# Kernel tuning notes

Measured on AMD Instinct MI355X. Metric: run time of the kernel, lower is better.

Reference implementation:

```python
import jax, jax.numpy as jnp
import numpy as np

B, NC, NT = 1, 128, 256
F = 8                       # fidnet filters (both 1h and 13c)
KH, KW = 5, 8               # fidnet kernel
DILS = [1, 2, 3, 4, 6, 8, 10, 12, 14, 16, 18, 20, 24, 28, 32]
BLOCKS = 3
L = BLOCKS * len(DILS)      # 45 wave layers per FIDNetLayer
RSTEPS, RK = 4, 9           # refine steps / refine kernel


def dfh_tanh(x):
    return jnp.tanh(x) * 0.98 + x * 0.02


def dfh_sigmoid(x):
    return jax.nn.sigmoid(x) * 0.98 + x * 0.02


def dfh_relu(x):
    return jax.nn.relu(x) * 0.98 + x * 0.02


def conv2d(x, w, b, dil_w=1, padding='VALID'):
    # x: NHWC, w: HWIO
    out = jax.lax.conv_general_dilated(x, w, (1, 1), padding,
                                       rhs_dilation=(1, dil_w),
                                       dimension_numbers=('NHWC', 'HWIO', 'NHWC'))
    return out + b


def hilbert(x):
    # analytic signal along last axis (real input, even length)
    N = x.shape[-1]
    hh = jnp.concatenate([jnp.ones(1, jnp.float32), 2.0 * jnp.ones(N // 2 - 1, jnp.float32),
                          jnp.ones(1, jnp.float32), jnp.zeros(N // 2 - 1, jnp.float32)]).astype(jnp.complex64)
    return jnp.fft.ifft(jnp.fft.fft(x.astype(jnp.complex64)) * hh)


def fidnet_layer(x, dw, db, wy1, by1, wy2, by2, wz0, bz0):
    # WaveNet-style stack of gated dilated convs with residuals + skip sum
    x = dfh_tanh(x @ dw + db)            # (B,H,W,2F)
    skip = jnp.zeros_like(x)
    ph = (KH - 1) // 2
    for i in range(wy1.shape[0]):
        dil = DILS[i % len(DILS)]
        xin = jnp.pad(x, ((0, 0), (ph, ph), (0, dil * (KW - 1)), (0, 0)))
        y1 = dfh_tanh(conv2d(xin, wy1[i], by1[i], dil))
        y2 = dfh_sigmoid(conv2d(xin, wy2[i], by2[i], dil))
        z = jnp.pad(y1 * y2, ((0, 0), (ph, ph), (0, KW - 1), (0, 0)))
        z = conv2d(z, wz0[i], bz0[i], 1)
        skip = skip + z
        x = z + x
    return dfh_tanh(skip)


def setup_inputs():
    key = jax.random.key(0)
    ks = jax.random.split(key, 16)
    n = lambda k, s, sc=0.05: jax.random.normal(k, s, jnp.float32) * sc
    return {
        'times': n(ks[0], (B, 2, NT), 1.0),
        'times_in': n(ks[1], (B, NC), 1.0),
        'inp_2d_nc': n(ks[2], (B, 1, NC, NT), 1.0),
        'inp_2d_c': n(ks[3], (B, 1, NC, NT), 1.0),
        'c_dense_w': n(ks[4], (4, 2 * F)), 'c_dense_b': jnp.zeros((2 * F,), jnp.float32),
        'c_wy1': n(ks[5], (L, KH, KW, 2 * F, F)), 'c_by1': jnp.zeros((L, F), jnp.float32),
        'c_wy2': n(ks[6], (L, KH, KW, 2 * F, F)), 'c_by2': jnp.zeros((L, F), jnp.float32),
        'c_wz0': n(ks[7], (L, KH, KW, F, 2 * F)), 'c_bz0': jnp.zeros((L, 2 * F), jnp.float32),
        'h_dense_w': n(ks[8], (2 * F, 2 * F)), 'h_dense_b': jnp.zeros((2 * F,), jnp.float32),
        'h_wy1': n(ks[9], (L, KH, KW, 2 * F, F)), 'h_by1': jnp.zeros((L, F), jnp.float32),
        'h_wy2': n(ks[10], (L, KH, KW, 2 * F, F)), 'h_by2': jnp.zeros((L, F), jnp.float32),
        'h_wz0': n(ks[11], (L, KH, KW, F, 2 * F)), 'h_bz0': jnp.zeros((L, 2 * F), jnp.float32),
        'ref_wr': n(ks[12], (RSTEPS, RK, RK, 8 * F, 4 * F), 0.02), 'ref_br': jnp.zeros((RSTEPS, 4 * F), jnp.float32),
        'ref_wt': n(ks[13], (RSTEPS, RK, RK, 8 * F, 4 * F), 0.02), 'ref_bt': jnp.zeros((RSTEPS, 4 * F), jnp.float32),
        'dense_w': n(ks[14], (12 * F, 2)), 'dense_b': jnp.zeros((2,), jnp.float32),
    }


def reference(times, times_in, inp_2d_nc, inp_2d_c,
              c_dense_w, c_dense_b, c_wy1, c_by1, c_wy2, c_by2, c_wz0, c_bz0,
              h_dense_w, h_dense_b, h_wy1, h_by1, h_wy2, h_by2, h_wz0, h_bz0,
              ref_wr, ref_br, ref_wt, ref_bt, dense_w, dense_b):
    Bn, _, nc, nt = inp_2d_nc.shape
    # build 4-channel input plane (B, NT, NC, 4)
    times_plane = jnp.tile(times[:, :1, :], (1, nc, 1))[:, None]          # (B,1,NC,NT)
    times_in_plane = jnp.tile(times_in[:, :, None], (1, 1, nt))[:, None]  # (B,1,NC,NT)
    tr = lambda a: jnp.transpose(a, (0, 3, 2, 1))
    inp = jnp.concatenate([tr(inp_2d_nc), tr(inp_2d_c), tr(times_plane), tr(times_in_plane)], axis=-1)

    cout = fidnet_layer(inp, c_dense_w, c_dense_b, c_wy1, c_by1, c_wy2, c_by2, c_wz0, c_bz0)  # (B,NT,NC,2F)
    cout = jnp.transpose(cout, (0, 3, 1, 2))               # (B,2F,NT,NC)
    cout = jnp.pad(cout, ((0, 0), (0, 0), (0, 0), (0, nc)))  # (B,2F,NT,2NC)
    mult = jnp.concatenate([jnp.full((1,), 0.5, jnp.float32), jnp.ones(nc - 1, jnp.float32)])
    multc = mult.astype(jnp.complex64)
    cout_ft = jnp.fft.fftshift(jnp.fft.fft(multc * (cout[..., 0::2] + 1j * cout[..., 1::2])), axes=-1)
    cout_ft = jnp.transpose(jnp.real(cout_ft), (0, 1, 3, 2))  # (B,2F,NC,NT)
    cout_ft = hilbert(cout_ft)
    hinp = jnp.conj(jnp.fft.fft(jnp.fft.fftshift(cout_ft, axes=-1)) / nt)
    mult_pad = jnp.pad(mult, (0, nt - nc), constant_values=1.0).astype(jnp.complex64)
    hinp = hinp / mult_pad
    zero_mask = jnp.where(jnp.abs(times[:, 0, 2::2]) > 0.0, 1.0, 0.0)
    zero_mask = jnp.pad(zero_mask, ((0, 0), (1, 0)), constant_values=1.0)[:, None, None, :]  # (B,1,1,NT//2)
    hinp = hinp[..., :nt // 2] * zero_mask
    hinp = jnp.stack([jnp.real(hinp), jnp.imag(hinp)], axis=-1).reshape(Bn, 2 * F, nc, nt)
    hinp = jnp.transpose(hinp, (0, 2, 3, 1)).astype(jnp.float32)  # (B,NC,NT,2F)

    hout = fidnet_layer(hinp, h_dense_w, h_dense_b, h_wy1, h_by1, h_wy2, h_by2, h_wz0, h_bz0)
    hout = jnp.concatenate([hout, hinp], axis=-1)          # (B,NC,NT,4F)
    hout = jnp.transpose(hout, (0, 3, 1, 2))               # (B,4F,NC,NT)
    hout = jnp.pad(hout, ((0, 0), (0, 0), (0, 0), (0, nt)))
    winH = jnp.concatenate([jnp.full((1,), 0.5, jnp.float32), jnp.ones(nt - 1, jnp.float32)]).astype(jnp.complex64)
    hout_ft = jnp.fft.fftshift(jnp.fft.fft(winH * (hout[..., 0::2] + 1j * hout[..., 1::2])), axes=-1)
    hout_ft = jnp.transpose(jnp.real(hout_ft), (0, 2, 3, 1))  # (B,NC,NT,4F)

    fnorm = jnp.max(jnp.abs(hout_ft), axis=(1, 2, 3), keepdims=True)
    ref = jnp.tile(hout_ft / fnorm, (1, 1, 1, 2))          # (B,NC,NT,8F)
    for i in range(ref_wr.shape[0]):
        rr = dfh_relu(conv2d(ref, ref_wr[i], ref_br[i], 1, 'SAME'))
        tt = dfh_tanh(conv2d(ref, ref_wt[i], ref_bt[i], 1, 'SAME'))
        ref = jnp.concatenate([tt, rr], axis=-1) + ref
    ref = ref * fnorm
    hfin = jnp.concatenate([ref, hout_ft], axis=-1) @ dense_w + dense_b  # (B,NC,NT,2)
    return jnp.stack([hfin[..., 0], hfin[..., 1] / fnorm[..., 0]], axis=-1)
```

## Files before the change

kernel.cpp:

```cpp
#include <hip/hip_runtime.h>

#define NTT 256
#define NCC 128

typedef __attribute__((ext_vector_type(8))) short bf16x8;
typedef __attribute__((ext_vector_type(4))) float f32x4;

__device__ __forceinline__ float dfh_tanh_f(float v){ return tanhf(v)*0.98f + 0.02f*v; }
__device__ __forceinline__ float dfh_sig_f(float v){ return 0.98f/(1.f+expf(-v)) + 0.02f*v; }
__device__ __forceinline__ unsigned f2bf(float x){
  unsigned u = __float_as_uint(x);
  return (u + 0x7fffu + ((u>>16)&1u)) >> 16;
}

__global__ __launch_bounds__(256) void k_build_c(
    const float* __restrict__ times, const float* __restrict__ times_in,
    const float* __restrict__ i2nc, const float* __restrict__ i2c,
    const float* __restrict__ dw, const float* __restrict__ db,
    float* __restrict__ x, unsigned short* __restrict__ xb,
    float* __restrict__ skip)
{
  int gid = blockIdx.x*256 + threadIdx.x;
  if (gid >= NTT*NCC) return;
  int c = gid & 127, t = gid >> 7;
  float v0 = i2nc[c*NTT + t];
  float v1 = i2c [c*NTT + t];
  float v2 = times[t];
  float v3 = times_in[c];
  #pragma unroll
  for (int f=0; f<16; ++f){
    float a = v0*dw[f] + v1*dw[16+f] + v2*dw[32+f] + v3*dw[48+f] + db[f];
    float xv = dfh_tanh_f(a);
    x[gid*16+f]    = xv;
    xb[gid*16+f]   = (unsigned short)f2bf(xv);
    skip[gid*16+f] = 0.f;
  }
}

__global__ __launch_bounds__(256) void k_build_h(
    const float* __restrict__ hinp, const float* __restrict__ dw,
    const float* __restrict__ db, float* __restrict__ x,
    unsigned short* __restrict__ xb, float* __restrict__ skip)
{
  int gid = blockIdx.x*256 + threadIdx.x;
  if (gid >= NCC*NTT) return;
  const float* in = hinp + gid*16;
  float iv[16];
  #pragma unroll
  for (int i=0;i<16;i++) iv[i]=in[i];
  #pragma unroll
  for (int f=0; f<16; ++f){
    float a = db[f];
    #pragma unroll
    for (int i=0;i<16;i++) a += iv[i]*dw[i*16+f];
    float xv = dfh_tanh_f(a);
    x[gid*16+f]    = xv;
    xb[gid*16+f]   = (unsigned short)f2bf(xv);
    skip[gid*16+f] = 0.f;
  }
}

__global__ __launch_bounds__(256) void k_wpack(
    const float* __restrict__ cwy1, const float* __restrict__ cwy2,
    const float* __restrict__ cwz0,
    const float* __restrict__ hwy1, const float* __restrict__ hwy2,
    const float* __restrict__ hwz0,
    unsigned short* __restrict__ gfrag, unsigned short* __restrict__ zfrag)
{
  int tid = blockIdx.x*256 + threadIdx.x;
  if (tid < 115200){
    int lane = tid & 63, ks = (tid>>6) % 20, layer = tid / 1280;
    const float* w1 = (layer < 45) ? cwy1 + layer*5120 : hwy1 + (layer-45)*5120;
    const float* w2 = (layer < 45) ? cwy2 + layer*5120 : hwy2 + (layer-45)*5120;
    int n = lane & 15;
    unsigned pk[4];
    #pragma unroll
    for (int jj=0; jj<4; ++jj){
      unsigned hl[2];
      #pragma unroll
      for (int h2=0; h2<2; ++h2){
        int k = ks*32 + (lane>>4)*8 + jj*2 + h2;
        int tap = k>>4, ci = k&15;
        float v = (n<8) ? w1[(tap*16+ci)*8 + n] : w2[(tap*16+ci)*8 + (n-8)];
        hl[h2] = f2bf(v);
      }
      pk[jj] = hl[0] | (hl[1]<<16);
    }
    uint4 v4; v4.x=pk[0]; v4.y=pk[1]; v4.z=pk[2]; v4.w=pk[3];
    *reinterpret_cast<uint4*>(gfrag + (size_t)tid*8) = v4;
  } else if (tid < 172800){
    int t2 = tid - 115200;
    int lane = t2 & 63, ks = (t2>>6) % 10, layer = t2 / 640;
    const float* wz = (layer < 45) ? cwz0 + layer*5120 : hwz0 + (layer-45)*5120;
    int n = lane & 15;
    unsigned pk[4];
    #pragma unroll
    for (int jj=0; jj<4; ++jj){
      unsigned hl[2];
      #pragma unroll
      for (int h2=0; h2<2; ++h2){
        int k = ks*32 + (lane>>4)*8 + jj*2 + h2;
        int tap = k>>3, ci = k&7;
        hl[h2] = f2bf(wz[(tap*8+ci)*16 + n]);
      }
      pk[jj] = hl[0] | (hl[1]<<16);
    }
    uint4 v4; v4.x=pk[0]; v4.y=pk[1]; v4.z=pk[2]; v4.w=pk[3];
    *reinterpret_cast<uint4*>(zfrag + (size_t)t2*8) = v4;
  }
}

template<int W>
__global__ __launch_bounds__(512) void k_gate_mfma(
    const unsigned short* __restrict__ xb, unsigned short* __restrict__ gb,
    const unsigned short* __restrict__ bfrag,
    const float* __restrict__ by1, const float* __restrict__ by2,
    int H, int dil)
{
  __shared__ __align__(16) unsigned short lds[(10*W+1)*8];
  const int tid = threadIdx.x, lane = tid & 63, wv = tid >> 6;
  const int nb = W/128;
  const int bid = blockIdx.x;
  const int wg = (bid & 7) * (gridDim.x >> 3) + (bid >> 3);
  const int h  = wg / nb;
  const int w0 = (wg % nb) * 128;
  const int NE = 10*W;

  bf16x8 bfr[20];
  #pragma unroll
  for (int ks = 0; ks < 20; ++ks)
    bfr[ks] = *reinterpret_cast<const bf16x8*>(bfrag + (ks*64 + lane)*8);

  for (int q = tid; q < NE; q += 512){
    int q2 = q >> 1, chunk = q & 1;
    int col = q2 % W, r = q2 / W;
    int hh = h + r - 2;
    uint4 v = make_uint4(0u,0u,0u,0u);
    if (hh >= 0 && hh < H)
      v = *reinterpret_cast<const uint4*>(xb + ((size_t)(hh*W+col))*16 + chunk*8);
    *reinterpret_cast<uint4*>(lds + ((r*2+chunk)*W + col)*8) = v;
  }
  if (tid == 0) *reinterpret_cast<uint4*>(lds + (size_t)NE*8) = make_uint4(0u,0u,0u,0u);
  __syncthreads();

  f32x4 acc0 = (f32x4){0.f,0.f,0.f,0.f};
  f32x4 acc1 = (f32x4){0.f,0.f,0.f,0.f};
  const int wbase = w0 + wv*16;
  const int zoff = NE*8;
  #pragma unroll
  for (int ks = 0; ks < 20; ++ks){
    int kh = ks >> 2, kw0 = (ks & 3)*2;
    if (w0 + dil*kw0 >= W) continue;
    int kw = kw0 + (lane>>5);
    int chunk = (lane>>4) & 1;
    int col = wbase + (lane&15) + dil*kw;
    int off = (col < W) ? ((kh*2+chunk)*W + col)*8 : zoff;
    bf16x8 a = *reinterpret_cast<const bf16x8*>(lds + off);
    if (ks & 1) acc1 = __builtin_amdgcn_mfma_f32_16x16x32_bf16(a, bfr[ks], acc1, 0,0,0);
    else        acc0 = __builtin_amdgcn_mfma_f32_16x16x32_bf16(a, bfr[ks], acc0, 0,0,0);
  }

  int n = lane & 15;
  float b1 = by1[n & 7], b2 = by2[n & 7];
  #pragma unroll
  for (int ri=0; ri<4; ++ri){
    float av = acc0[ri] + acc1[ri];
    float own = av + b1;
    float oth = __shfl_xor(av, 8) + b2;
    if (n < 8){
      float gv = dfh_tanh_f(own) * dfh_sig_f(oth);
      int w = wbase + (lane>>4)*4 + ri;
      gb[((size_t)(h*W + w))*8 + n] = (unsigned short)f2bf(gv);
    }
  }
}

template<int W>
__global__ __launch_bounds__(512) void k_zres_mfma(
    const unsigned short* __restrict__ gb,
    float* __restrict__ x, unsigned short* __restrict__ xb,
    float* __restrict__ skip,
    const unsigned short* __restrict__ bfrag,
    const float* __restrict__ bz, int H)
{
  __shared__ __align__(16) unsigned short lds[(5*W+1)*8];
  const int tid = threadIdx.x, lane = tid & 63, wv = tid >> 6;
  const int nb = W/128;
  const int bid = blockIdx.x;
  const int wg = (bid & 7) * (gridDim.x >> 3) + (bid >> 3);
  const int h  = wg / nb;
  const int w0 = (wg % nb) * 128;

  bf16x8 bfr[10];
  #pragma unroll
  for (int ks = 0; ks < 10; ++ks)
    bfr[ks] = *reinterpret_cast<const bf16x8*>(bfrag + (ks*64 + lane)*8);

  for (int q = tid; q < 5*W; q += 512){
    int col = q % W, r = q / W;
    int hh = h + r - 2;
    uint4 v = make_uint4(0u,0u,0u,0u);
    if (hh >= 0 && hh < H)
      v = *reinterpret_cast<const uint4*>(gb + ((size_t)(hh*W+col))*8);
    *reinterpret_cast<uint4*>(lds + (r*W+col)*8) = v;
  }
  if (tid == 0) *reinterpret_cast<uint4*>(lds + (size_t)(5*W)*8) = make_uint4(0u,0u,0u,0u);
  __syncthreads();

  f32x4 acc0 = (f32x4){0.f,0.f,0.f,0.f};
  f32x4 acc1 = (f32x4){0.f,0.f,0.f,0.f};
  const int wbase = w0 + wv*16;
  const int zoff = 5*W*8;
  #pragma unroll
  for (int ks = 0; ks < 10; ++ks){
    int kh = ks >> 1, kw = (ks & 1)*4 + (lane>>4);
    int col = wbase + (lane&15) + kw;
    int off = (col < W) ? (kh*W + col)*8 : zoff;
    bf16x8 a = *reinterpret_cast<const bf16x8*>(lds + off);
    if (ks & 1) acc1 = __builtin_amdgcn_mfma_f32_16x16x32_bf16(a, bfr[ks], acc1, 0,0,0);
    else        acc0 = __builtin_amdgcn_mfma_f32_16x16x32_bf16(a, bfr[ks], acc0, 0,0,0);
  }

  int n = lane & 15;
  float bv = bz[n];
  #pragma unroll
  for (int ri=0; ri<4; ++ri){
    int w = wbase + (lane>>4)*4 + ri;
    size_t idx = ((size_t)(h*W + w))*16 + n;
    float z = acc0[ri] + acc1[ri] + bv;
    skip[idx] += z;
    float xn = x[idx] + z;
    x[idx]  = xn;
    xb[idx] = (unsigned short)f2bf(xn);
  }
}

__global__ __launch_bounds__(256) void k_dtanh_t(const float* __restrict__ s,
                                                 float* __restrict__ o)
{
  __shared__ float tile[256][17];
  int c = blockIdx.x;
  int tid = threadIdx.x;
  int f = tid & 15, tq = tid >> 4;
  #pragma unroll
  for (int p = 0; p < 16; ++p){
    int t = p*16 + tq;
    tile[t][f] = s[((size_t)t*128 + c)*16 + f];
  }
  __syncthreads();
  int t = tid;
  #pragma unroll
  for (int f2 = 0; f2 < 16; ++f2)
    o[(size_t)f2*32768 + c*256 + t] = dfh_tanh_f(tile[t][f2]);
}

__global__ __launch_bounds__(256) void k_dft_c1(const float* __restrict__ cout,
                                                float* __restrict__ cft)
{
  __shared__ float ctab[128], stab[128];
  int tid = threadIdx.x;
  if (tid < 128){
    float ang = (float)tid * (6.283185307179586f/128.f);
    ctab[tid] = cosf(ang); stab[tid] = sinf(ang);
  }
  __syncthreads();
  int gid = blockIdx.x*256 + tid;
  int t = gid & 255, c = (gid>>8)&127, f = gid>>15;
  int j = (c + 64) & 127;
  const float* base = cout + (size_t)f*32768 + t;
  float acc = 0.5f*base[0];
  for (int k=1; k<64; ++k){
    float re = base[(2*k)*256], im = base[(2*k+1)*256];
    int m = (j*k) & 127;
    acc += re*ctab[m] + im*stab[m];
  }
  cft[(f*128 + c)*256 + t] = acc;
}

__global__ __launch_bounds__(256) void k_dft_c2(const float* __restrict__ cft,
                                                const float* __restrict__ times,
                                                float* __restrict__ hinp)
{
  __shared__ float ctab[256], stab[256];
  int tid = threadIdx.x;
  {
    float ang = (float)tid * (6.283185307179586f/256.f);
    ctab[tid] = cosf(ang); stab[tid] = sinf(ang);
  }
  __syncthreads();
  int gid = blockIdx.x*256 + tid;
  int k = gid & 127, c = (gid>>7)&127, f = gid>>14;
  const float* r = cft + (f*128 + c)*256;
  float ar = 0.f, as = 0.f;
  for (int t=0; t<256; ++t){
    float rv = r[t];
    int m = (k*t) & 255;
    ar += rv*ctab[m];
    as += rv*stab[m];
  }
  float q;
  if (k == 0) q = 1.f/128.f;
  else {
    float mk = (fabsf(times[2*k]) > 0.f) ? 1.f : 0.f;
    q = ((k & 1) ? -1.f : 1.f) * (1.f/128.f) * mk;
  }
  float* o = hinp + (c*256 + 2*k)*16 + f;
  o[0]  = q*ar;
  o[16] = q*as;
}

__global__ __launch_bounds__(256) void k_houtcat(const float* __restrict__ skip,
                                                 const float* __restrict__ hinp,
                                                 float* __restrict__ hc,
                                                 unsigned* __restrict__ fb)
{
  int gid = blockIdx.x*256 + threadIdx.x;
  if (gid == 0) *fb = 0u;
  if (gid >= NCC*NTT) return;
  #pragma unroll
  for (int f=0; f<16; ++f){
    hc[gid*32 + f]      = dfh_tanh_f(skip[gid*16+f]);
    hc[gid*32 + 16 + f] = hinp[gid*16+f];
  }
}

__global__ __launch_bounds__(256) void k_dft_e(const float* __restrict__ hc,
                                               float* __restrict__ hft)
{
  __shared__ float ctab[256], stab[256];
  int tid = threadIdx.x;
  {
    float ang = (float)tid * (6.283185307179586f/256.f);
    ctab[tid] = cosf(ang); stab[tid] = sinf(ang);
  }
  __syncthreads();
  int gid = blockIdx.x*256 + tid;
  int f = gid & 31, t = (gid>>5)&255, c = gid>>13;
  int j = (t + 128) & 255;
  const float* base = hc + c*(256*32) + f;
  float acc = 0.5f*base[0];
  for (int k=1; k<128; ++k){
    float re = base[(2*k)*32], im = base[(2*k+1)*32];
    int m = (j*k) & 255;
    acc += re*ctab[m] + im*stab[m];
  }
  hft[(c*256 + t)*32 + f] = acc;
}

__global__ __launch_bounds__(256) void k_fnorm(const float* __restrict__ hft,
                                               unsigned* __restrict__ fb, int n)
{
  float m = 0.f;
  for (int i = blockIdx.x*256 + threadIdx.x; i < n; i += gridDim.x*256)
    m = fmaxf(m, fabsf(hft[i]));
  #pragma unroll
  for (int off=32; off>0; off>>=1) m = fmaxf(m, __shfl_down(m, off));
  if ((threadIdx.x & 63) == 0) atomicMax(fb, __float_as_uint(m));
}

__global__ __launch_bounds__(256) void k_refinit(const float* __restrict__ hft,
                                                 const unsigned* __restrict__ fb,
                                                 float* __restrict__ ref)
{
  int gid = blockIdx.x*256 + threadIdx.x;
  if (gid >= NCC*NTT*64) return;
  float fn = __uint_as_float(*fb);
  int f = gid & 63, ct = gid >> 6;
  ref[gid] = hft[ct*32 + (f & 31)] / fn;
}

__global__ __launch_bounds__(256) void k_wconv4(
    const float* __restrict__ wt0, const float* __restrict__ wr0,
    unsigned short* __restrict__ bfrag)
{
  int gid = blockIdx.x*256 + threadIdx.x;
  if (gid >= 4*648*64) return;
  int step = gid / 41472, rem = gid % 41472;
  int lane = rem & 63, frag = rem >> 6;
  int nt = frag & 3, kt = (frag>>2) & 1, p = frag >> 3;
  const float* wt = wt0 + step*165888;
  const float* wr = wr0 + step*165888;
  int o = nt*16 + (lane & 15);
  int ci0 = kt*32 + (lane>>4)*8;
  const float* src = (o < 32) ? (wt + (p*64 + ci0)*32 + o)
                              : (wr + (p*64 + ci0)*32 + (o-32));
  unsigned pk[4];
  #pragma unroll
  for (int j=0;j<4;++j)
    pk[j] = f2bf(src[(2*j)*32]) | (f2bf(src[(2*j+1)*32]) << 16);
  uint4 v; v.x = pk[0]; v.y = pk[1]; v.z = pk[2]; v.w = pk[3];
  *reinterpret_cast<uint4*>(bfrag + (size_t)gid*8) = v;
}

__device__ __forceinline__ void ref_stage_load2(const float* __restrict__ srcf,
    int c, int kh, int t0, int tid, float4 (&fr)[2][2])
{
  int cc = c + kh - 4;
  #pragma unroll
  for (int r2=0; r2<2; ++r2){
    float4 z = make_float4(0.f,0.f,0.f,0.f);
    fr[r2][0] = z; fr[r2][1] = z;
    int q = tid + r2*256;
    if (q < 320){
      int row = q >> 3, c16 = q & 7;
      int t = t0 - 4 + row;
      if (t >= 0 && t < 256){
        const float* sp = srcf + ((size_t)(cc*256 + t))*64 + c16*8;
        fr[r2][0] = *reinterpret_cast<const float4*>(sp);
        fr[r2][1] = *reinterpret_cast<const float4*>(sp + 4);
      }
    }
  }
}

__device__ __forceinline__ void ref_stage_write2(unsigned short* lds,
    int tid, float4 (&fr)[2][2])
{
  #pragma unroll
  for (int r2=0; r2<2; ++r2){
    int q = tid + r2*256;
    if (q < 320){
      int row = q >> 3, c16 = q & 7;
      uint4 v;
      v.x = f2bf(fr[r2][0].x) | (f2bf(fr[r2][0].y)<<16);
      v.y = f2bf(fr[r2][0].z) | (f2bf(fr[r2][0].w)<<16);
      v.z = f2bf(fr[r2][1].x) | (f2bf(fr[r2][1].y)<<16);
      v.w = f2bf(fr[r2][1].z) | (f2bf(fr[r2][1].w)<<16);
      *reinterpret_cast<uint4*>(&lds[row*64 + ((c16 ^ (row&7))*8)]) = v;
    }
  }
}

__global__ __launch_bounds__(256) void k_refmfma(
    const float* __restrict__ srcf, float* __restrict__ dstf,
    const unsigned short* __restrict__ bfrag,
    const float* __restrict__ bt, const float* __restrict__ br)
{
  __shared__ __align__(16) unsigned short ldsA[2][40*64];
  __shared__ float redbuf[2][16][65];
  const int tid = threadIdx.x, lane = tid & 63, wv = tid >> 6;
  const int mt = wv & 1, kt = wv >> 1;
  int bid = blockIdx.x;
  int wg = (bid & 7)*128 + (bid >> 3);
  const int c  = wg >> 3;
  const int t0 = (wg & 7) * 32;

  f32x4 acc[4];
  #pragma unroll
  for (int nt=0; nt<4; ++nt) acc[nt] = (f32x4){0.f,0.f,0.f,0.f};

  const int kh0 = (c < 4)   ? 4 - c   : 0;
  const int kh1 = (c > 123) ? 131 - c : 8;

  float4 fr[2][2];
  ref_stage_load2(srcf, c, kh0, t0, tid, fr);
  int cur = 0;
  for (int kh = kh0; kh <= kh1; ++kh){
    ref_stage_write2(ldsA[cur], tid, fr);
    __syncthreads();
    if (kh < kh1) ref_stage_load2(srcf, c, kh+1, t0, tid, fr);
    for (int kw=0; kw<9; ++kw){
      const int p = kh*9 + kw;
      const unsigned short* bb = bfrag + (size_t)p*4096;
      bf16x8 b[4];
      #pragma unroll
      for (int nt=0; nt<4; ++nt)
        b[nt] = *reinterpret_cast<const bf16x8*>(bb + ((kt*4+nt)*64 + lane)*8);
      const int j = mt*16 + (lane&15) + kw;
      bf16x8 a = *reinterpret_cast<const bf16x8*>(
          &ldsA[cur][j*64 + (((kt*4 + (lane>>4)) ^ (j&7))*8)]);
      #pragma unroll
      for (int nt=0; nt<4; ++nt)
        acc[nt] = __builtin_amdgcn_mfma_f32_16x16x32_bf16(a, b[nt], acc[nt], 0,0,0);
    }
    __syncthreads();
    cur ^= 1;
  }

  if (kt == 1){
    #pragma unroll
    for (int nt=0; nt<4; ++nt)
      #pragma unroll
      for (int ri=0; ri<4; ++ri)
        redbuf[mt][nt*4+ri][lane] = acc[nt][ri];
  }
  __syncthreads();
  if (kt == 0){
    #pragma unroll
    for (int nt=0; nt<4; ++nt){
      int o = nt*16 + (lane&15);
      float bv = (o < 32) ? bt[o] : br[o-32];
      #pragma unroll
      for (int ri=0; ri<4; ++ri){
        int t = t0 + mt*16 + (lane>>4)*4 + ri;
        float v = acc[nt][ri] + redbuf[mt][nt*4+ri][lane] + bv;
        v = (nt < 2) ? dfh_tanh_f(v) : (v > 0.f ? v : 0.02f*v);
        size_t idx = ((size_t)(c*256 + t))*64 + o;
        dstf[idx] = v + srcf[idx];
      }
    }
  }
}

__global__ __launch_bounds__(256) void k_final(const float* __restrict__ ref,
                                               const float* __restrict__ hft,
                                               const unsigned* __restrict__ fb,
                                               const float* __restrict__ dw,
                                               const float* __restrict__ db,
                                               float* __restrict__ out)
{
  int gid = blockIdx.x*256 + threadIdx.x;
  if (gid >= NCC*NTT) return;
  float fn = __uint_as_float(*fb);
  const float* rp = ref + gid*64;
  const float* hp = hft + gid*32;
  float s0 = db[0], s1 = db[1];
  #pragma unroll 8
  for (int f=0; f<64; ++f){ float v = rp[f]*fn; s0 += v*dw[f*2]; s1 += v*dw[f*2+1]; }
  #pragma unroll 8
  for (int f=0; f<32; ++f){ float v = hp[f]; s0 += v*dw[(64+f)*2]; s1 += v*dw[(64+f)*2+1]; }
  out[gid*2]   = s0;
  out[gid*2+1] = s1/fn;
}

extern "C" void kernel_launch(void* const* d_in, const int* in_sizes, int n_in,
                              void* d_out, int out_size, void* d_ws, size_t ws_size,
                              hipStream_t stream)
{
  const float* times    = (const float*)d_in[0];
  const float* times_in = (const float*)d_in[1];
  const float* i2nc     = (const float*)d_in[2];
  const float* i2c      = (const float*)d_in[3];
  const float* cdw  = (const float*)d_in[4];  const float* cdb  = (const float*)d_in[5];
  const float* cwy1 = (const float*)d_in[6];  const float* cby1 = (const float*)d_in[7];
  const float* cwy2 = (const float*)d_in[8];  const float* cby2 = (const float*)d_in[9];
  const float* cwz0 = (const float*)d_in[10]; const float* cbz0 = (const float*)d_in[11];
  const float* hdw  = (const float*)d_in[12]; const float* hdb  = (const float*)d_in[13];
  const float* hwy1 = (const float*)d_in[14]; const float* hby1 = (const float*)d_in[15];
  const float* hwy2 = (const float*)d_in[16]; const float* hby2 = (const float*)d_in[17];
  const float* hwz0 = (const float*)d_in[18]; const float* hbz0 = (const float*)d_in[19];
  const float* rwr  = (const float*)d_in[20]; const float* rbr  = (const float*)d_in[21];
  const float* rwt  = (const float*)d_in[22]; const float* rbt  = (const float*)d_in[23];
  const float* fdw  = (const float*)d_in[24]; const float* fdb  = (const float*)d_in[25];
  float* out = (float*)d_out;

  float* ws = (float*)d_ws;
  float* A   = ws;
  float* Bb  = ws + 524288;
  float* C   = ws + 1048576;
  unsigned short* xb = (unsigned short*)(ws + 1572864);
  unsigned short* gb = (unsigned short*)(ws + 1835008);
  float* hcat = ws + 1966080;
  float* hft  = ws + 3014656;
  unsigned short* gfrag  = (unsigned short*)(ws + 4146176);
  unsigned short* zfrag  = (unsigned short*)(ws + 4606976);
  float* refA = ws;
  unsigned short* bfrag4 = (unsigned short*)(ws + 2097152);
  float* refB = ws + 4146176;
  unsigned* fb = (unsigned*)(ws + 6243328);

  float* x_c = A;  float* skp_c = Bb; float* cout = C;
  float* cft = A;  float* hinp  = Bb; float* x_h  = C; float* skp_h = A;

  static const int DILS[15] = {1,2,3,4,6,8,10,12,14,16,18,20,24,28,32};

  k_wpack<<<675,256,0,stream>>>(cwy1, cwy2, cwz0, hwy1, hwy2, hwz0, gfrag, zfrag);

  k_build_c<<<128,256,0,stream>>>(times, times_in, i2nc, i2c, cdw, cdb, x_c, xb, skp_c);
  for (int i=0; i<45; ++i){
    int dil = DILS[i % 15];
    k_gate_mfma<128><<<256,512,0,stream>>>(xb, gb, gfrag + (size_t)i*10240,
                                           cby1 + i*8, cby2 + i*8, 256, dil);
    k_zres_mfma<128><<<256,512,0,stream>>>(gb, x_c, xb, skp_c, zfrag + (size_t)i*5120,
                                           cbz0 + i*16, 256);
  }
  k_dtanh_t<<<128,256,0,stream>>>(skp_c, cout);

  k_dft_c1<<<2048,256,0,stream>>>(cout, cft);
  k_dft_c2<<<1024,256,0,stream>>>(cft, times, hinp);

  k_build_h<<<128,256,0,stream>>>(hinp, hdw, hdb, x_h, xb, skp_h);
  for (int i=0; i<45; ++i){
    int dil = DILS[i % 15];
    k_gate_mfma<256><<<256,512,0,stream>>>(xb, gb, gfrag + (size_t)(45+i)*10240,
                                           hby1 + i*8, hby2 + i*8, 128, dil);
    k_zres_mfma<256><<<256,512,0,stream>>>(gb, x_h, xb, skp_h, zfrag + (size_t)(45+i)*5120,
                                           hbz0 + i*16, 128);
  }
  k_houtcat<<<128,256,0,stream>>>(skp_h, hinp, hcat, fb);

  k_dft_e<<<4096,256,0,stream>>>(hcat, hft);
  k_fnorm<<<1024,256,0,stream>>>(hft, fb, 1048576);

  k_wconv4<<<648,256,0,stream>>>(rwt, rwr, bfrag4);
  k_refinit<<<8192,256,0,stream>>>(hft, fb, refA);
  float* rsrc = refA; float* rdst = refB;
  for (int i=0; i<4; ++i){
    k_refmfma<<<1024,256,0,stream>>>(rsrc, rdst, bfrag4 + (size_t)i*331776,
                                     rbt + i*32, rbr + i*32);
    float* tmp = rsrc; rsrc = rdst; rdst = tmp;
  }

  k_final<<<128,256,0,stream>>>(rsrc, hft, fb, fdw, fdb, out);
}
```

Baseline: 1.295 ms.

## Fuse z-residual of each wave layer with the next layer's gate convolution

```diff
diff --git a/kernel.cpp b/kernel.cpp
--- a/kernel.cpp
+++ b/kernel.cpp
@@ -232,6 +232,119 @@
     float xn = x[idx] + z;
     x[idx]  = xn;
     xb[idx] = (unsigned short)f2bf(xn);
+  }
+}
+
+template<int W, int H, int NBW>
+__global__ __launch_bounds__(512) void k_zg(
+    const unsigned short* __restrict__ gbsrc, unsigned short* __restrict__ gbdst,
+    const float* __restrict__ xsrc, float* __restrict__ xdst,
+    float* __restrict__ skip,
+    const unsigned short* __restrict__ zfrag, const float* __restrict__ bz,
+    const unsigned short* __restrict__ gfrag,
+    const float* __restrict__ by1, const float* __restrict__ by2,
+    int dil)
+{
+  __shared__ __align__(16) unsigned short ldsG[(9*W+1)*8];
+  __shared__ __align__(16) unsigned short xl[5*W*16 + 8];
+  const int tid = threadIdx.x, lane = tid & 63, wv = tid >> 6;
+  const int bid = blockIdx.x;
+  const int wg = (bid & 7) * (gridDim.x >> 3) + (bid >> 3);
+  const int h  = wg / NBW;
+  const int w0 = (wg % NBW) * 128;
+
+  bf16x8 zb[10];
+  #pragma unroll
+  for (int ks = 0; ks < 10; ++ks)
+    zb[ks] = *reinterpret_cast<const bf16x8*>(zfrag + (ks*64 + lane)*8);
+
+  for (int q = tid; q < 9*W; q += 512){
+    int col = q % W, r = q / W;
+    int hh = h + r - 4;
+    uint4 v = make_uint4(0u,0u,0u,0u);
+    if (hh >= 0 && hh < H)
+      v = *reinterpret_cast<const uint4*>(gbsrc + ((size_t)(hh*W+col))*8);
+    *reinterpret_cast<uint4*>(ldsG + (r*W+col)*8) = v;
+  }
+  if (tid == 0){
+    *reinterpret_cast<uint4*>(ldsG + (size_t)(9*W)*8) = make_uint4(0u,0u,0u,0u);
+    *reinterpret_cast<uint4*>(xl + (size_t)5*W*16) = make_uint4(0u,0u,0u,0u);
+  }
+  if (h < 2 || h >= H-2){
+    for (int q = tid; q < 5*W*2; q += 512)
+      *reinterpret_cast<uint4*>(xl + (size_t)q*8) = make_uint4(0u,0u,0u,0u);
+  }
+  __syncthreads();
+
+  const int zoffG = 9*W*8;
+  const int NT = 5*(W/16);
+  for (int tt = wv; tt < NT; tt += 8){
+    int d  = tt / (W/16), ct = tt % (W/16);
+    int hr = h - 2 + d;
+    if (hr < 0 || hr >= H) continue;
+    int wt = ct*16;
+    f32x4 a0 = (f32x4){0.f,0.f,0.f,0.f};
+    f32x4 a1 = (f32x4){0.f,0.f,0.f,0.f};
+    #pragma unroll
+    for (int ks = 0; ks < 10; ++ks){
+      int kh = ks >> 1, kw = (ks & 1)*4 + (lane>>4);
+      int col = wt + (lane&15) + kw;
+      int off = (col < W) ? ((d+kh)*W + col)*8 : zoffG;
+      bf16x8 a = *reinterpret_cast<const bf16x8*>(ldsG + off);
+      if (ks & 1) a1 = __builtin_amdgcn_mfma_f32_16x16x32_bf16(a, zb[ks], a1, 0,0,0);
+      else        a0 = __builtin_amdgcn_mfma_f32_16x16x32_bf16(a, zb[ks], a0, 0,0,0);
+    }
+    int n = lane & 15;
+    float bv = bz[n];
+    #pragma unroll
+    for (int ri=0; ri<4; ++ri){
+      int w = wt + (lane>>4)*4 + ri;
+      size_t idx = ((size_t)(hr*W + w))*16 + n;
+      float z = a0[ri] + a1[ri] + bv;
+      float xn = xsrc[idx] + z;
+      xl[(d*W + w)*16 + n] = (unsigned short)f2bf(xn);
+      if (d == 2 && (w & ~127) == w0){
+        skip[idx] += z;
+        xdst[idx] = xn;
+      }
+    }
+  }
+  __syncthreads();
+
+  bf16x8 gb2[20];
+  #pragma unroll
+  for (int ks = 0; ks < 20; ++ks)
+    gb2[ks] = *reinterpret_cast<const bf16x8*>(gfrag + (ks*64 + lane)*8);
+
+  const int zoffX = 5*W*16;
+  const int wbase = w0 + wv*16;
+  f32x4 acc0 = (f32x4){0.f,0.f,0.f,0.f};
+  f32x4 acc1 = (f32x4){0.f,0.f,0.f,0.f};
+  #pragma unroll
+  for (int ks = 0; ks < 20; ++ks){
+    int kh = ks >> 2, kw0 = (ks & 3)*2;
+    if (wbase + dil*kw0 >= W) continue;
+    int kw = kw0 + (lane>>5);
+    int chunk = (lane>>4) & 1;
+    int col = wbase + (lane&15) + dil*kw;
+    int off = (col < W) ? ((kh*W + col)*16 + chunk*8) : zoffX;
+    bf16x8 a = *reinterpret_cast<const bf16x8*>(xl + off);
+    if (ks & 1) acc1 = __builtin_amdgcn_mfma_f32_16x16x32_bf16(a, gb2[ks], acc1, 0,0,0);
+    else        acc0 = __builtin_amdgcn_mfma_f32_16x16x32_bf16(a, gb2[ks], acc0, 0,0,0);
+  }
+
+  int n = lane & 15;
+  float b1 = by1[n & 7], b2 = by2[n & 7];
+  #pragma unroll
+  for (int ri=0; ri<4; ++ri){
+    float av = acc0[ri] + acc1[ri];
+    float own = av + b1;
+    float oth = __shfl_xor(av, 8) + b2;
+    if (n < 8){
+      float gv = dfh_tanh_f(own) * dfh_sig_f(oth);
+      int w = wbase + (lane>>4)*4 + ri;
+      gbdst[((size_t)(h*W + w))*8 + n] = (unsigned short)f2bf(gv);
+    }
   }
 }
 
@@ -549,9 +662,11 @@
   float* Bb  = ws + 524288;
   float* C   = ws + 1048576;
   unsigned short* xb = (unsigned short*)(ws + 1572864);
-  unsigned short* gb = (unsigned short*)(ws + 1835008);
+  unsigned short* gbA = (unsigned short*)(ws + 1835008);
   float* hcat = ws + 1966080;
+  float* xB   = ws + 1966080;
   float* hft  = ws + 3014656;
+  unsigned short* gbB = (unsigned short*)(ws + 3014656);
   unsigned short* gfrag  = (unsigned short*)(ws + 4146176);
   unsigned short* zfrag  = (unsigned short*)(ws + 4606976);
   float* refA = ws;
@@ -567,26 +682,39 @@
   k_wpack<<<675,256,0,stream>>>(cwy1, cwy2, cwz0, hwy1, hwy2, hwz0, gfrag, zfrag);
 
   k_build_c<<<128,256,0,stream>>>(times, times_in, i2nc, i2c, cdw, cdb, x_c, xb, skp_c);
-  for (int i=0; i<45; ++i){
-    int dil = DILS[i % 15];
-    k_gate_mfma<128><<<256,512,0,stream>>>(xb, gb, gfrag + (size_t)i*10240,
-                                           cby1 + i*8, cby2 + i*8, 256, dil);
-    k_zres_mfma<128><<<256,512,0,stream>>>(gb, x_c, xb, skp_c, zfrag + (size_t)i*5120,
-                                           cbz0 + i*16, 256);
-  }
+  k_gate_mfma<128><<<256,512,0,stream>>>(xb, gbA, gfrag, cby1, cby2, 256, DILS[0]);
+  for (int i=0; i<44; ++i){
+    const float* xs = (i & 1) ? xB  : x_c;
+    float*       xd = (i & 1) ? x_c : xB;
+    const unsigned short* gs = (i & 1) ? gbB : gbA;
+    unsigned short*       gd = (i & 1) ? gbA : gbB;
+    k_zg<128,256,1><<<256,512,0,stream>>>(gs, gd, xs, xd, skp_c,
+        zfrag + (size_t)i*5120, cbz0 + i*16,
+        gfrag + (size_t)(i+1)*10240, cby1 + (i+1)*8, cby2 + (i+1)*8,
+        DILS[(i+1) % 15]);
+  }
+  k_zres_mfma<128><<<256,512,0,stream>>>(gbA, x_c, xb, skp_c,
+      zfrag + (size_t)44*5120, cbz0 + 44*16, 256);
   k_dtanh_t<<<128,256,0,stream>>>(skp_c, cout);
 
   k_dft_c1<<<2048,256,0,stream>>>(cout, cft);
   k_dft_c2<<<1024,256,0,stream>>>(cft, times, hinp);
 
   k_build_h<<<128,256,0,stream>>>(hinp, hdw, hdb, x_h, xb, skp_h);
-  for (int i=0; i<45; ++i){
-    int dil = DILS[i % 15];
-    k_gate_mfma<256><<<256,512,0,stream>>>(xb, gb, gfrag + (size_t)(45+i)*10240,
-                                           hby1 + i*8, hby2 + i*8, 128, dil);
-    k_zres_mfma<256><<<256,512,0,stream>>>(gb, x_h, xb, skp_h, zfrag + (size_t)(45+i)*5120,
-                                           hbz0 + i*16, 128);
-  }
+  k_gate_mfma<256><<<256,512,0,stream>>>(xb, gbA, gfrag + (size_t)45*10240,
+                                         hby1, hby2, 128, DILS[0]);
+  for (int i=0; i<44; ++i){
+    const float* xs = (i & 1) ? xB  : x_h;
+    float*       xd = (i & 1) ? x_h : xB;
+    const unsigned short* gs = (i & 1) ? gbB : gbA;
+    unsigned short*       gd = (i & 1) ? gbA : gbB;
+    k_zg<256,128,2><<<256,512,0,stream>>>(gs, gd, xs, xd, skp_h,
+        zfrag + (size_t)(45+i)*5120, hbz0 + i*16,
+        gfrag + (size_t)(45+i+1)*10240, hby1 + (i+1)*8, hby2 + (i+1)*8,
+        DILS[(i+1) % 15]);
+  }
+  k_zres_mfma<256><<<256,512,0,stream>>>(gbA, x_h, xb, skp_h,
+      zfrag + (size_t)(45+44)*5120, hbz0 + 44*16, 128);
   k_houtcat<<<128,256,0,stream>>>(skp_h, hinp, hcat, fb);
 
   k_dft_e<<<4096,256,0,stream>>>(hcat, hft);
```

Result: slower. 1.599 ms (+23.5%).
